# Optimization experiments

Hardware: AMD Instinct MI355X
Metric: run time of the kernel (lower is better)

The kernel has to match this reference:

```python
import jax, jax.numpy as jnp
import numpy as np

EMPTY = -1  # sentinel for empty (vertex, region) slots, as in the TF layer


def setup_inputs() -> dict:
    key = jax.random.key(0)
    m, vertices, regions = 128, 2048, 32
    # values in [-1, vertices): -1 marks an empty slot, otherwise a vertex id
    mapping = jax.random.randint(key, (m, vertices, regions), EMPTY, vertices, dtype=jnp.int32)
    return {"mapping": mapping}


def reference(mapping):
    """Faithful JAX version of Graph2Col.call.

    TF's tf.where(mask) emits coordinates of True entries in row-major order
    with a data-dependent row count. For jit-compatibility we emit a
    fixed-size [m*V*R, ...] result where valid entries come first (same
    row-major order as tf.where) and padding rows are filled with -1.
    """
    m, V, R = mapping.shape
    total = m * V * R
    flat_map = mapping.reshape(-1)                 # [total]
    # row index is never -1, so the reduce_all mask is simply mapping != -1
    flat_mask = flat_map != EMPTY                  # [total] bool

    # stable stream compaction: valid entries first, preserving row-major order
    order = jnp.argsort(~flat_mask)                # stable sort -> tf.where ordering
    valid = flat_mask[order]                       # [total] bool

    rows = order // (V * R)
    rem = order % (V * R)
    verts = rem // R
    regs = rem % R

    # column_indices: coordinates of non-empty slots (tf.where returns int64)
    column_indices = jnp.stack([rows, verts, regs], axis=-1).astype(jnp.int64)  # [total, 3]
    # nodes_indices: (batch_row, vertex_id) gathered at those coordinates (int32)
    nodes_indices = jnp.stack([rows.astype(jnp.int32), flat_map[order]], axis=-1)  # [total, 2]

    column_indices = jnp.where(valid[:, None], column_indices, jnp.int64(EMPTY))
    nodes_indices = jnp.where(valid[:, None], nodes_indices, jnp.int32(EMPTY))
    return nodes_indices, column_indices
```

## Files before the change

kernel.cpp:

```cpp
#include <hip/hip_runtime.h>


#define EMPTY_V (-1)

constexpr int M_DIM = 128;
constexpr int V_DIM = 2048;
constexpr int R_DIM = 32;
constexpr int TOTAL = M_DIM * V_DIM * R_DIM;
constexpr int BLOCK = 256;
constexpr int CHUNK = 8192;
constexpr int NB = TOTAL / CHUNK;
constexpr int SUBT = CHUNK / (BLOCK * 4);
constexpr int NWAVE = BLOCK / 64;

__global__ __launch_bounds__(BLOCK) void k_count(const int* __restrict__ in,
                                                 int* __restrict__ counts) {
    const int b = blockIdx.x;
    const int tid = threadIdx.x;
    const int4* p = (const int4*)(in + (size_t)b * CHUNK);
    int c = 0;
#pragma unroll
    for (int s = 0; s < SUBT; ++s) {
        int4 v = p[s * BLOCK + tid];
        c += (v.x != EMPTY_V) + (v.y != EMPTY_V) + (v.z != EMPTY_V) + (v.w != EMPTY_V);
    }
    for (int d = 32; d > 0; d >>= 1) c += __shfl_down(c, d, 64);
    __shared__ int ws[NWAVE];
    const int lane = tid & 63, wid = tid >> 6;
    if (lane == 0) ws[wid] = c;
    __syncthreads();
    if (tid == 0) {
        int t = 0;
        for (int w = 0; w < NWAVE; ++w) t += ws[w];
        counts[b] = t;
    }
}

__global__ __launch_bounds__(NB) void k_scan(const int* __restrict__ counts,
                                             int* __restrict__ offsets,
                                             int* __restrict__ total_valid) {
    const int tid = threadIdx.x;
    const int lane = tid & 63, wid = tid >> 6;
    int c = counts[tid];
    int incl = c;
    for (int d = 1; d < 64; d <<= 1) {
        int y = __shfl_up(incl, d, 64);
        if (lane >= d) incl += y;
    }
    __shared__ int ws[NB / 64];
    if (lane == 63) ws[wid] = incl;
    __syncthreads();
    int woff = 0;
    for (int w = 0; w < wid; ++w) woff += ws[w];
    offsets[tid] = woff + incl - c;
    if (tid == NB - 1) *total_valid = woff + incl;
}

__global__ __launch_bounds__(BLOCK) void k_scatter(const int* __restrict__ in,
                                                   const int* __restrict__ offsets,
                                                   int* __restrict__ out_nodes,
                                                   int* __restrict__ out_cols) {
    const int b = blockIdx.x;
    const int tid = threadIdx.x;
    const int lane = tid & 63, wid = tid >> 6;
    const unsigned long long below = (lane == 0) ? 0ull : ((~0ull) >> (64 - lane));
    __shared__ int wsum[SUBT][NWAVE];
    int running = offsets[b];
    const int4* p = (const int4*)(in + (size_t)b * CHUNK);
#pragma unroll
    for (int s = 0; s < SUBT; ++s) {
        int4 v = p[s * BLOCK + tid];
        const int f0 = (v.x != EMPTY_V), f1 = (v.y != EMPTY_V);
        const int f2 = (v.z != EMPTY_V), f3 = (v.w != EMPTY_V);
        const unsigned long long b0 = __ballot(f0), b1 = __ballot(f1);
        const unsigned long long b2 = __ballot(f2), b3 = __ballot(f3);
        const int pre = __popcll(b0 & below) + __popcll(b1 & below) +
                        __popcll(b2 & below) + __popcll(b3 & below);
        const int wtot = __popcll(b0) + __popcll(b1) + __popcll(b2) + __popcll(b3);
        if (lane == 0) wsum[s][wid] = wtot;
        __syncthreads();
        int woff = 0, stot = 0;
        for (int w = 0; w < NWAVE; ++w) {
            const int x = wsum[s][w];
            stot += x;
            if (w < wid) woff += x;
        }
        int pos = running + woff + pre;
        const int i0 = b * CHUNK + s * (BLOCK * 4) + tid * 4;
        const int vals[4] = {v.x, v.y, v.z, v.w};
#pragma unroll
        for (int j = 0; j < 4; ++j) {
            if (vals[j] != EMPTY_V) {
                const int fi = i0 + j;
                const int row = fi >> 16;
                const int rem = fi & 65535;
                const int vert = rem >> 5;
                const int reg = rem & 31;
                out_nodes[2 * pos]     = row;
                out_nodes[2 * pos + 1] = vals[j];
                out_cols[3 * pos]      = row;
                out_cols[3 * pos + 1]  = vert;
                out_cols[3 * pos + 2]  = reg;
                ++pos;
            }
        }
        running += stot;
    }
}

__global__ __launch_bounds__(BLOCK) void k_tail(const int* __restrict__ total_valid,
                                                int* __restrict__ out_nodes,
                                                int* __restrict__ out_cols) {
    const int tv = *total_valid;
    const int stride = gridDim.x * blockDim.x;
    for (int pos = tv + blockIdx.x * blockDim.x + threadIdx.x; pos < TOTAL;
         pos += stride) {
        out_nodes[2 * pos]     = EMPTY_V;
        out_nodes[2 * pos + 1] = EMPTY_V;
        out_cols[3 * pos]      = EMPTY_V;
        out_cols[3 * pos + 1]  = EMPTY_V;
        out_cols[3 * pos + 2]  = EMPTY_V;
    }
}

extern "C" void kernel_launch(void* const* d_in, const int* in_sizes, int n_in,
                              void* d_out, int out_size, void* d_ws, size_t ws_size,
                              hipStream_t stream) {
    const int* in = (const int*)d_in[0];
    int* out = (int*)d_out;
    int* out_nodes = out;
    int* out_cols = out + 2 * (size_t)TOTAL;
    int* ws = (int*)d_ws;
    int* counts = ws;
    int* offsets = ws + NB;
    int* tv = ws + 2 * NB;

    k_count<<<NB, BLOCK, 0, stream>>>(in, counts);
    k_scan<<<1, NB, 0, stream>>>(counts, offsets, tv);
    k_scatter<<<NB, BLOCK, 0, stream>>>(in, offsets, out_nodes, out_cols);
    k_tail<<<512, BLOCK, 0, stream>>>(tv, out_nodes, out_cols);
}
```

Measured before the change: 212.3 us.

## Stage compacted entries in LDS and write outputs with coalesced stores

The scatter kernel now writes each subtile's compacted values and positions into shared memory, then has the block write the node and column outputs contiguously. The old code issued scattered per-thread scalar stores. Node pairs go out as int2, and column triples are emitted dword-by-dword across threads. This adds two extra barriers per subtile, LDS traffic, and a divide by 3, and it disables unrolling of the subtile loop.

```diff
diff --git a/kernel.cpp b/kernel.cpp
--- a/kernel.cpp
+++ b/kernel.cpp
@@ -12,6 +12,7 @@
 constexpr int NB = TOTAL / CHUNK;
 constexpr int SUBT = CHUNK / (BLOCK * 4);
 constexpr int NWAVE = BLOCK / 64;
+constexpr int STAGE = BLOCK * 4;
 
 __global__ __launch_bounds__(BLOCK) void k_count(const int* __restrict__ in,
                                                  int* __restrict__ counts) {
@@ -63,13 +64,16 @@
     const int b = blockIdx.x;
     const int tid = threadIdx.x;
     const int lane = tid & 63, wid = tid >> 6;
-    const unsigned long long below = (lane == 0) ? 0ull : ((~0ull) >> (64 - lane));
-    __shared__ int wsum[SUBT][NWAVE];
+    const unsigned long long below = lane ? ((~0ull) >> (64 - lane)) : 0ull;
+    __shared__ int wsum[NWAVE];
+    __shared__ int s_val[STAGE];
+    __shared__ int s_pos[STAGE];
+    const int row = b >> 3;
     int running = offsets[b];
     const int4* p = (const int4*)(in + (size_t)b * CHUNK);
-#pragma unroll
+#pragma unroll 1
     for (int s = 0; s < SUBT; ++s) {
-        int4 v = p[s * BLOCK + tid];
+        const int4 v = p[s * BLOCK + tid];
         const int f0 = (v.x != EMPTY_V), f1 = (v.y != EMPTY_V);
         const int f2 = (v.z != EMPTY_V), f3 = (v.w != EMPTY_V);
         const unsigned long long b0 = __ballot(f0), b1 = __ballot(f1);
@@ -77,34 +81,41 @@
         const int pre = __popcll(b0 & below) + __popcll(b1 & below) +
                         __popcll(b2 & below) + __popcll(b3 & below);
         const int wtot = __popcll(b0) + __popcll(b1) + __popcll(b2) + __popcll(b3);
-        if (lane == 0) wsum[s][wid] = wtot;
+        if (lane == 0) wsum[wid] = wtot;
         __syncthreads();
-        int woff = 0, stot = 0;
+        int woff = 0, cnt = 0;
         for (int w = 0; w < NWAVE; ++w) {
-            const int x = wsum[s][w];
-            stot += x;
+            const int x = wsum[w];
+            cnt += x;
             if (w < wid) woff += x;
         }
-        int pos = running + woff + pre;
-        const int i0 = b * CHUNK + s * (BLOCK * 4) + tid * 4;
+        int lp = woff + pre;
+        const int rem0 = ((b & 7) << 13) + (s << 10) + (tid << 2);
         const int vals[4] = {v.x, v.y, v.z, v.w};
+        const int fl[4] = {f0, f1, f2, f3};
 #pragma unroll
         for (int j = 0; j < 4; ++j) {
-            if (vals[j] != EMPTY_V) {
-                const int fi = i0 + j;
-                const int row = fi >> 16;
-                const int rem = fi & 65535;
-                const int vert = rem >> 5;
-                const int reg = rem & 31;
-                out_nodes[2 * pos]     = row;
-                out_nodes[2 * pos + 1] = vals[j];
-                out_cols[3 * pos]      = row;
-                out_cols[3 * pos + 1]  = vert;
-                out_cols[3 * pos + 2]  = reg;
-                ++pos;
+            if (fl[j]) { s_val[lp] = vals[j]; s_pos[lp] = rem0 + j; ++lp; }
+        }
+        __syncthreads();
+        int2* ndst2 = (int2*)(out_nodes + 2 * (size_t)running);
+        for (int k = tid; k < cnt; k += BLOCK) {
+            ndst2[k] = make_int2(row, s_val[k]);
+        }
+        int* cdst = out_cols + 3 * (size_t)running;
+        const int cdw = 3 * cnt;
+        for (int d = tid; d < cdw; d += BLOCK) {
+            const int e = d / 3;
+            const int r = d - 3 * e;
+            int val = row;
+            if (r != 0) {
+                const int pp = s_pos[e];
+                val = (r == 1) ? (pp >> 5) : (pp & 31);
             }
+            cdst[d] = val;
         }
-        running += stot;
+        running += cnt;
+        __syncthreads();
     }
 }
 
```

Result: faster. 196.7 us (-7.4%).
